# Performance work log

Hardware: AMD Instinct MI355X
Metric: run time of the kernel (lower is better)

Reference implementation:

```python
import jax, jax.numpy as jnp
import numpy as np

B, L, C, H, W = 2, 3, 64, 32, 32
DI, N, DT_RANK, K = 128, 16, 4, 4  # d_inner=2*C, d_state, dt_rank=ceil(C/16), 4 scan dirs


def setup_inputs() -> dict:
    key = jax.random.key(0)
    ks = iter(jax.random.split(key, 48))
    nrm = lambda shape, s=0.02: jax.random.normal(next(ks), shape, jnp.float32) * s
    return {
        "image_sequence": jax.random.normal(next(ks), (B, L, C, H, W), jnp.float32),
        "difficult_zone": jax.random.normal(next(ks), (B, C, H, W), jnp.float32),
        "sigma": jax.random.uniform(next(ks), (B, C, H, W), jnp.float32),
        # LayerNorm2d applied to each frame
        "norm_g": jnp.ones((C,)), "norm_b": jnp.zeros((C,)),
        # ConvolutionalResBlock (in=3C -> out=C), GroupNorm(num_groups=1)
        "gn1_g": jnp.ones((3 * C,)), "gn1_b": jnp.zeros((3 * C,)),
        "conv1_w": nrm((C, 3 * C, 3, 3)), "conv1_b": jnp.zeros((C,)),
        "gn2_g": jnp.ones((C,)), "gn2_b": jnp.zeros((C,)),
        "conv2_w": nrm((C, C, 3, 3)), "conv2_b": jnp.zeros((C,)),
        "skip_w": nrm((C, 3 * C, 1, 1)), "skip_b": jnp.zeros((C,)),
        # VSSBlock pre-norms
        "ln1_g": jnp.ones((C,)), "ln1_b": jnp.zeros((C,)),
        "ln2_g": jnp.ones((C,)), "ln2_b": jnp.zeros((C,)),
        # SS2D
        "in_proj_w": nrm((2 * DI, C)),
        "dwconv_w": nrm((DI, 1, 3, 3)), "dwconv_b": jnp.zeros((DI,)),
        "x_proj_w": nrm((K, DT_RANK + 2 * N, DI)),
        "dt_proj_w": nrm((K, DI, DT_RANK), 0.1),
        "dt_proj_b": jnp.log(jnp.expm1(jnp.full((K, DI), 0.01, jnp.float32))),
        "A_logs": jnp.log(jnp.tile(jnp.arange(1, N + 1, dtype=jnp.float32), (K * DI, 1))),
        "Ds": jnp.ones((K * DI,)),
        "out_norm_g": jnp.ones((DI,)), "out_norm_b": jnp.zeros((DI,)),
        "out_proj_w": nrm((C, DI)),
        # Mlp (hidden = C)
        "fc1_w": nrm((C, C)), "fc1_b": jnp.zeros((C,)),
        "fc2_w": nrm((C, C)), "fc2_b": jnp.zeros((C,)),
    }


def _ln(x, g, b, eps=1e-5):  # layernorm over last axis
    m = x.mean(-1, keepdims=True)
    v = x.var(-1, keepdims=True)
    return (x - m) * jax.lax.rsqrt(v + eps) * g + b


def _ln2d(x, g, b, eps=1e-6):  # per-pixel channel layernorm, NCHW
    m = x.mean(1, keepdims=True)
    v = x.var(1, keepdims=True)
    return (x - m) * jax.lax.rsqrt(v + eps) * g[None, :, None, None] + b[None, :, None, None]


def _gn1(x, g, b, eps=1e-5):  # GroupNorm(num_groups=1), NCHW
    m = x.mean((1, 2, 3), keepdims=True)
    v = x.var((1, 2, 3), keepdims=True)
    return (x - m) * jax.lax.rsqrt(v + eps) * g[None, :, None, None] + b[None, :, None, None]


def _conv(x, w, b, pad):
    y = jax.lax.conv_general_dilated(x, w, (1, 1), [(pad, pad), (pad, pad)],
                                     dimension_numbers=("NCHW", "OIHW", "NCHW"))
    return y + b[None, :, None, None]


def _forward(image_sequence, difficult_zone, sigma, norm_g, norm_b, gn1_g, gn1_b,
             conv1_w, conv1_b, gn2_g, gn2_b, conv2_w, conv2_b, skip_w, skip_b,
             ln1_g, ln1_b, ln2_g, ln2_b, in_proj_w, dwconv_w, dwconv_b, x_proj_w,
             dt_proj_w, dt_proj_b, A_logs, Ds, out_norm_g, out_norm_b, out_proj_w,
             fc1_w, fc1_b, fc2_w, fc2_b):
    b, l, c, h, w = image_sequence.shape
    bl, L2 = b * l, h * w
    # fold frame loop into batch (identical math per frame in the torch loop)
    frames = _ln2d(image_sequence.reshape(bl, c, h, w), norm_g, norm_b)
    dz = jnp.broadcast_to(difficult_zone[:, None], (b, l, c, h, w)).reshape(bl, c, h, w)
    sg = jnp.broadcast_to(sigma[:, None], (b, l, c, h, w)).reshape(bl, c, h, w)
    x = jnp.concatenate([dz, frames, sg], axis=1)  # [bl, 3c, h, w]
    # channel compressor: pre-act conv res block
    hdn = _conv(jax.nn.silu(_gn1(x, gn1_g, gn1_b)), conv1_w, conv1_b, 1)
    hdn = _conv(jax.nn.silu(_gn1(hdn, gn2_g, gn2_b)), conv2_w, conv2_b, 1)
    x = hdn + _conv(x, skip_w, skip_b, 0)          # [bl, c, h, w]
    x = x.transpose(0, 2, 3, 1)                    # [bl, h, w, c]
    # --- VSSBlock (pre-norm): x = x + SS2D(LN(x)) ---
    xn = _ln(x, ln1_g, ln1_b)
    xz = xn @ in_proj_w.T                          # [bl,h,w,2*DI]
    xc, z = jnp.split(xz, 2, axis=-1)
    xc = xc.transpose(0, 3, 1, 2)                  # [bl, DI, h, w]
    xc = jax.lax.conv_general_dilated(xc, dwconv_w, (1, 1), [(1, 1), (1, 1)],
                                      dimension_numbers=("NCHW", "OIHW", "NCHW"),
                                      feature_group_count=DI) + dwconv_b[None, :, None, None]
    xc = jax.nn.silu(xc)
    # 4-direction scan inputs (HW, WH, and their reverses)
    xf = xc.reshape(bl, DI, L2)
    xt = xc.transpose(0, 1, 3, 2).reshape(bl, DI, L2)
    xs = jnp.stack([xf, xt], axis=1)
    xs = jnp.concatenate([xs, jnp.flip(xs, axis=-1)], axis=1)  # [bl, 4, DI, L2]
    x_dbl = jnp.einsum("bkdl,kcd->bkcl", xs, x_proj_w)
    dts, Bs, Cs = jnp.split(x_dbl, [DT_RANK, DT_RANK + N], axis=2)
    dts = jnp.einsum("bkrl,kdr->bkdl", dts, dt_proj_w) + dt_proj_b[None, :, :, None]
    dts = jax.nn.softplus(dts)                     # [bl, 4, DI, L2]
    A = -jnp.exp(A_logs).reshape(K, DI, N)
    dA = jnp.exp(dts[..., None] * A[None, :, :, None, :])            # [bl,4,DI,L2,N]
    dBu = dts[..., None] * Bs.transpose(0, 1, 3, 2)[:, :, None] * xs[..., None]
    a_t = dA.transpose(3, 0, 1, 2, 4)              # [L2, bl, 4, DI, N]
    bu_t = dBu.transpose(3, 0, 1, 2, 4)
    c_t = Cs.transpose(3, 0, 1, 2)                 # [L2, bl, 4, N]

    def step(hid, inp):
        a_i, bu_i, c_i = inp
        hid = a_i * hid + bu_i
        return hid, jnp.einsum("bkdn,bkn->bkd", hid, c_i)

    h0 = jnp.zeros((bl, K, DI, N), xs.dtype)
    _, ys = jax.lax.scan(step, h0, (a_t, bu_t, c_t))                 # [L2, bl, 4, DI]
    ys = ys.transpose(1, 2, 3, 0) + xs * Ds.reshape(K, DI)[None, :, :, None]
    inv = jnp.flip(ys[:, 2:4], axis=-1)
    y = (ys[:, 0] + inv[:, 0]
         + ys[:, 1].reshape(bl, DI, w, h).transpose(0, 1, 3, 2).reshape(bl, DI, L2)
         + inv[:, 1].reshape(bl, DI, w, h).transpose(0, 1, 3, 2).reshape(bl, DI, L2))
    y = _ln(y.transpose(0, 2, 1), out_norm_g, out_norm_b).reshape(bl, h, w, DI)
    y = y * jax.nn.silu(z)
    x = x + y @ out_proj_w.T
    # --- x = x + Mlp(LN(x)) ---
    xn = _ln(x, ln2_g, ln2_b)
    x = x + (jax.nn.gelu(xn @ fc1_w.T + fc1_b, approximate=False) @ fc2_w.T + fc2_b)
    return x.transpose(0, 3, 1, 2).reshape(b, l, c, h, w)


def reference(image_sequence, difficult_zone, sigma, norm_g, norm_b, gn1_g, gn1_b,
              conv1_w, conv1_b, gn2_g, gn2_b, conv2_w, conv2_b, skip_w, skip_b,
              ln1_g, ln1_b, ln2_g, ln2_b, in_proj_w, dwconv_w, dwconv_b, x_proj_w,
              dt_proj_w, dt_proj_b, A_logs, Ds, out_norm_g, out_norm_b, out_proj_w,
              fc1_w, fc1_b, fc2_w, fc2_b):
    return _forward(image_sequence, difficult_zone, sigma, norm_g, norm_b, gn1_g, gn1_b,
                    conv1_w, conv1_b, gn2_g, gn2_b, conv2_w, conv2_b, skip_w, skip_b,
                    ln1_g, ln1_b, ln2_g, ln2_b, in_proj_w, dwconv_w, dwconv_b, x_proj_w,
                    dt_proj_w, dt_proj_b, A_logs, Ds, out_norm_g, out_norm_b, out_proj_w,
                    fc1_w, fc1_b, fc2_w, fc2_b)
```

## Files before the change

kernel.cpp:

```cpp
#include <hip/hip_runtime.h>
#include <math.h>

#define BL    6
#define CCH   64
#define C3    192
#define L2    1024
#define DIC   128
#define NST   16
#define K4    4
#define PSTR  1088
#define NCH   32

#define LOG2E 1.44269504088896340736f
#define LN2C  0.69314718055994530942f

__device__ __forceinline__ float fexp(float x){ return __builtin_amdgcn_exp2f(x*LOG2E); }
__device__ __forceinline__ float fsilu(float x){ return x / (1.f + fexp(-x)); }
__device__ __forceinline__ float fsoftplus(float x){
  if (x > 20.f) return x;
  return __builtin_amdgcn_logf(1.f + fexp(x)) * LN2C;
}
__device__ __forceinline__ float fgelu(float x){
  return 0.5f*x*(1.f + erff(x*0.70710678118654752440f));
}

__global__ __launch_bounds__(256) void k_ln2d(const float* __restrict__ img,
    const float* __restrict__ dz, const float* __restrict__ sg,
    const float* __restrict__ g, const float* __restrict__ b, float* __restrict__ x3c){
  __shared__ float ps[4][64], pq[4][64];
  int s = blockIdx.x >> 4;
  int lane = threadIdx.x & 63;
  int cg = threadIdx.x >> 6;
  int p = ((blockIdx.x & 15) << 6) + lane;
  int bsmp = s/3;
  const float* fr = img + (size_t)s*CCH*L2;
  float vals[16]; float sm=0.f, sq=0.f;
  #pragma unroll
  for (int j=0;j<16;++j){
    int c = cg*16+j;
    float v = fr[c*L2+p];
    vals[j]=v; sm+=v; sq+=v*v;
  }
  ps[cg][lane]=sm; pq[cg][lane]=sq;
  __syncthreads();
  sm = ps[0][lane]+ps[1][lane]+ps[2][lane]+ps[3][lane];
  sq = pq[0][lane]+pq[1][lane]+pq[2][lane]+pq[3][lane];
  float mean = sm*(1.f/CCH); float var = sq*(1.f/CCH) - mean*mean;
  float rs = rsqrtf(var + 1e-6f);
  float* o = x3c + (size_t)s*C3*L2;
  const float* dzp = dz + (size_t)bsmp*CCH*L2;
  const float* sgp = sg + (size_t)bsmp*CCH*L2;
  #pragma unroll
  for (int j=0;j<16;++j){
    int c = cg*16+j;
    o[c*L2+p] = dzp[c*L2+p];
    o[(CCH+c)*L2+p] = (vals[j]-mean)*rs*g[c] + b[c];
    o[(2*CCH+c)*L2+p] = sgp[c*L2+p];
  }
}

__global__ __launch_bounds__(256) void k_gnstats_part(const float* __restrict__ x,
    int elems_per_s, float* __restrict__ psum, float* __restrict__ psq){
  int s = blockIdx.x >> 4; int i = blockIdx.x & 15;
  int chunk = elems_per_s >> 4;
  int tid = threadIdx.x;
  const float* xs = x + (size_t)s*elems_per_s + (size_t)i*chunk;
  float sm=0.f, sq=0.f;
  for (int idx = tid*4; idx < chunk; idx += 1024){
    float4 v = *(const float4*)(xs+idx);
    sm += v.x+v.y+v.z+v.w;
    sq += v.x*v.x+v.y*v.y+v.z*v.z+v.w*v.w;
  }
  for (int m=1;m<64;m<<=1){ sm+=__shfl_xor(sm,m,64); sq+=__shfl_xor(sq,m,64); }
  __shared__ float s_sm[4], s_sq[4];
  int wv = tid>>6;
  if ((tid&63)==0){ s_sm[wv]=sm; s_sq[wv]=sq; }
  __syncthreads();
  if (tid==0){
    psum[s*16+i] = s_sm[0]+s_sm[1]+s_sm[2]+s_sm[3];
    psq [s*16+i] = s_sq[0]+s_sq[1]+s_sq[2]+s_sq[3];
  }
}

__global__ __launch_bounds__(64) void k_gnstats_final(const float* __restrict__ psum,
    const float* __restrict__ psq, int elems_per_s, float eps, float* __restrict__ stats){
  int s = blockIdx.x; int lane = threadIdx.x;
  float sm = lane<16 ? psum[s*16+lane] : 0.f;
  float sq = lane<16 ? psq [s*16+lane] : 0.f;
  for (int m=1;m<16;m<<=1){ sm+=__shfl_xor(sm,m,64); sq+=__shfl_xor(sq,m,64); }
  if (lane==0){
    float mean = sm/elems_per_s; float var = sq/elems_per_s - mean*mean;
    stats[s*2] = mean; stats[s*2+1] = rsqrtf(var+eps);
  }
}

__global__ __launch_bounds__(256) void k_gnact_pad(const float* __restrict__ x,
    const float* __restrict__ stats, const float* __restrict__ g, const float* __restrict__ b,
    int ch, float* __restrict__ out){
  int bx = blockIdx.x;
  int s = bx / ch; int c = bx % ch;
  int tid = threadIdx.x;
  float mean = stats[s*2], rs = stats[s*2+1];
  float gc = g[c]*rs; float bc = b[c] - mean*rs*g[c];
  float4 v = *(const float4*)(x + (size_t)bx*1024 + tid*4);
  float4 o; o.x = fsilu(v.x*gc+bc); o.y = fsilu(v.y*gc+bc);
  o.z = fsilu(v.z*gc+bc); o.w = fsilu(v.w*gc+bc);
  float* pl = out + (size_t)bx*PSTR;
  *(float4*)(pl + 32 + tid*4) = o;
  float4 z4 = make_float4(0.f,0.f,0.f,0.f);
  if (tid < 8)  *(float4*)(pl + tid*4) = z4;
  else if (tid < 16) *(float4*)(pl + 1056 + (tid-8)*4) = z4;
}

__device__ __forceinline__ void conv_row_acc(float4& a0, float4& a1, float4 mid, float lf, float rt,
    const float* wp0, const float* wp1){
  float w0=wp0[0], w1=wp0[1], w2=wp0[2];
  a0.x = fmaf(w0,lf,   fmaf(w1,mid.x, fmaf(w2,mid.y, a0.x)));
  a0.y = fmaf(w0,mid.x,fmaf(w1,mid.y, fmaf(w2,mid.z, a0.y)));
  a0.z = fmaf(w0,mid.y,fmaf(w1,mid.z, fmaf(w2,mid.w, a0.z)));
  a0.w = fmaf(w0,mid.z,fmaf(w1,mid.w, fmaf(w2,rt,    a0.w)));
  float v0=wp1[0], v1=wp1[1], v2=wp1[2];
  a1.x = fmaf(v0,lf,   fmaf(v1,mid.x, fmaf(v2,mid.y, a1.x)));
  a1.y = fmaf(v0,mid.x,fmaf(v1,mid.y, fmaf(v2,mid.z, a1.y)));
  a1.z = fmaf(v0,mid.y,fmaf(v1,mid.z, fmaf(v2,mid.w, a1.z)));
  a1.w = fmaf(v0,mid.z,fmaf(v1,mid.w, fmaf(v2,rt,    a1.w)));
}

__device__ __forceinline__ void conv_ci_body(float4 m0, float4 m1, float4 m2, int q,
    const float* wp0, const float* wp1, float4& a0, float4& a1){
  float lf0=__shfl_up(m0.w,1,64), rt0=__shfl_down(m0.x,1,64);
  float lf1=__shfl_up(m1.w,1,64), rt1=__shfl_down(m1.x,1,64);
  float lf2=__shfl_up(m2.w,1,64), rt2=__shfl_down(m2.x,1,64);
  if (q==0){ lf0=0.f; lf1=0.f; lf2=0.f; }
  if (q==7){ rt0=0.f; rt1=0.f; rt2=0.f; }
  conv_row_acc(a0,a1,m0,lf0,rt0, wp0+0, wp1+0);
  conv_row_acc(a0,a1,m1,lf1,rt1, wp0+3, wp1+3);
  conv_row_acc(a0,a1,m2,lf2,rt2, wp0+6, wp1+6);
}

__global__ __launch_bounds__(256) void k_conv1_split(const float* __restrict__ xact,
    const float* __restrict__ w, float* __restrict__ part){
  int bx = blockIdx.x; int kk = bx&7; int cop=(bx>>3)&31; int s=bx>>8;
  int co0 = cop*2, co1 = co0+1;
  int tid = threadIdx.x; int row = tid>>3; int q = tid&7; int col0 = q*4;
  float4 a0 = make_float4(0.f,0.f,0.f,0.f);
  float4 a1 = make_float4(0.f,0.f,0.f,0.f);
  int ci0 = kk*24;
  const float* pl = xact + ((size_t)s*C3 + ci0)*PSTR + row*32 + col0;
  const float* wp0 = w + (size_t)(co0*C3 + ci0)*9;
  const float* wp1 = w + (size_t)(co1*C3 + ci0)*9;
  float4 m0 = *(const float4*)(pl);
  float4 m1 = *(const float4*)(pl+32);
  float4 m2 = *(const float4*)(pl+64);
  #pragma unroll 2
  for (int i=0;i<24;++i){
    const float* pn = pl + (i<23 ? PSTR : 0);
    float4 n0 = *(const float4*)(pn);
    float4 n1 = *(const float4*)(pn+32);
    float4 n2 = *(const float4*)(pn+64);
    conv_ci_body(m0,m1,m2,q, wp0, wp1, a0, a1);
    wp0 += 9; wp1 += 9; pl = pn; m0=n0; m1=n1; m2=n2;
  }
  float* pp = part + (size_t)kk*(BL*CCH*L2) + ((size_t)s*CCH+co0)*L2 + row*32+col0;
  *(float4*)pp = a0;
  *(float4*)(pp+L2) = a1;
}

__global__ __launch_bounds__(256) void k_reduce1(const float* __restrict__ part,
    const float* __restrict__ bias, float* __restrict__ h1){
  int co = blockIdx.x & 63; int s = blockIdx.x >> 6;
  size_t ofs = ((size_t)s*CCH+co)*L2 + threadIdx.x*4;
  const size_t stride = (size_t)BL*CCH*L2;
  float4 acc = *(const float4*)(part + ofs);
  #pragma unroll
  for (int kk=1;kk<8;++kk){
    float4 r = *(const float4*)(part + (size_t)kk*stride + ofs);
    acc.x += r.x; acc.y += r.y; acc.z += r.z; acc.w += r.w;
  }
  float bv = bias[co];
  acc.x += bv; acc.y += bv; acc.z += bv; acc.w += bv;
  *(float4*)(h1 + ofs) = acc;
}

__global__ __launch_bounds__(256) void k_conv2_split(const float* __restrict__ xact2,
    const float* __restrict__ x3c, const float* __restrict__ w2,
    const float* __restrict__ wsk, float* __restrict__ part){
  int t = blockIdx.x; int role = t % 3; t /= 3;
  int cop = t & 31; int s = t >> 5;
  int co0 = cop*2, co1 = co0+1;
  int tid = threadIdx.x; int row = tid>>3; int q = tid&7; int col0 = q*4;
  int p = row*32+col0;
  float4 a0 = make_float4(0.f,0.f,0.f,0.f);
  float4 a1 = make_float4(0.f,0.f,0.f,0.f);
  if (role < 2){
    int ci0 = role*32;
    const float* pl = xact2 + ((size_t)s*CCH + ci0)*PSTR + row*32 + col0;
    const float* wp0 = w2 + (size_t)(co0*CCH + ci0)*9;
    const float* wp1 = w2 + (size_t)(co1*CCH + ci0)*9;
    float4 m0 = *(const float4*)(pl);
    float4 m1 = *(const float4*)(pl+32);
    float4 m2 = *(const float4*)(pl+64);
    #pragma unroll 2
    for (int i=0;i<32;++i){
      const float* pn = pl + (i<31 ? PSTR : 0);
      float4 n0 = *(const float4*)(pn);
      float4 n1 = *(const float4*)(pn+32);
      float4 n2 = *(const float4*)(pn+64);
      conv_ci_body(m0,m1,m2,q, wp0, wp1, a0, a1);
      wp0 += 9; wp1 += 9; pl = pn; m0=n0; m1=n1; m2=n2;
    }
  } else {
    const float* x3 = x3c + (size_t)s*C3*L2 + p;
    #pragma unroll 4
    for (int ci=0; ci<C3; ++ci){
      float4 v = *(const float4*)(x3 + (size_t)ci*L2);
      float ws0 = wsk[co0*C3+ci], ws1 = wsk[co1*C3+ci];
      a0.x = fmaf(ws0,v.x,a0.x); a0.y = fmaf(ws0,v.y,a0.y); a0.z = fmaf(ws0,v.z,a0.z); a0.w = fmaf(ws0,v.w,a0.w);
      a1.x = fmaf(ws1,v.x,a1.x); a1.y = fmaf(ws1,v.y,a1.y); a1.z = fmaf(ws1,v.z,a1.z); a1.w = fmaf(ws1,v.w,a1.w);
    }
  }
  float* pp = part + (size_t)role*(BL*CCH*L2) + ((size_t)s*CCH+co0)*L2 + p;
  *(float4*)pp = a0;
  *(float4*)(pp+L2) = a1;
}

__global__ __launch_bounds__(256) void k_reduce2(const float* __restrict__ part,
    const float* __restrict__ b2, const float* __restrict__ bsk,
    float* __restrict__ xp, float* __restrict__ x_cmaj){
  int co = blockIdx.x & 63; int s = blockIdx.x >> 6;
  int p = threadIdx.x*4;
  size_t ofs = ((size_t)s*CCH+co)*L2 + p;
  const size_t stride = (size_t)BL*CCH*L2;
  float4 r0 = *(const float4*)(part + ofs);
  float4 r1 = *(const float4*)(part + stride + ofs);
  float4 r2 = *(const float4*)(part + 2*stride + ofs);
  float bv = b2[co]+bsk[co];
  float4 o;
  o.x = r0.x+r1.x+r2.x+bv;
  o.y = r0.y+r1.y+r2.y+bv;
  o.z = r0.z+r1.z+r2.z+bv;
  o.w = r0.w+r1.w+r2.w+bv;
  *(float4*)(x_cmaj + ofs) = o;
  float* xpb = xp + ((size_t)s*L2 + p)*CCH + co;
  xpb[0] = o.x; xpb[CCH] = o.y; xpb[2*CCH] = o.z; xpb[3*CCH] = o.w;
}

__global__ __launch_bounds__(256) void k_ln1_inproj(const float* __restrict__ xp,
    const float* __restrict__ g, const float* __restrict__ b, const float* __restrict__ W,
    float* __restrict__ xc, float* __restrict__ z_t){
  __shared__ float xn_s[64*65];
  int bx = blockIdx.x; int oq = bx & 3; int pg = (bx>>2)&15; int s = bx>>6;
  int p0 = pg*64;
  int tid = threadIdx.x; int wv = __builtin_amdgcn_readfirstlane(tid>>6); int lane = tid&63;
  for (int j=0;j<16;++j){
    int pl = wv*16 + j; int p = p0 + pl;
    float v = xp[((size_t)s*L2 + p)*CCH + lane];
    float sm = v, sq = v*v;
    for (int m=1;m<64;m<<=1){ sm += __shfl_xor(sm,m,64); sq += __shfl_xor(sq,m,64); }
    float mean = sm*(1.f/64.f); float var = sq*(1.f/64.f) - mean*mean;
    float rs = rsqrtf(var + 1e-5f);
    xn_s[pl*65 + lane] = (v-mean)*rs*g[lane] + b[lane];
  }
  __syncthreads();
  int px_l = tid & 63;
  int og = __builtin_amdgcn_readfirstlane(tid >> 6);
  int o0 = oq*64 + og*16;
  float acc[16];
  #pragma unroll
  for (int oi=0;oi<16;++oi) acc[oi]=0.f;
  for (int c=0;c<64;++c){
    float xv = xn_s[px_l*65 + c];
    #pragma unroll
    for (int oi=0;oi<16;++oi) acc[oi] = fmaf(W[(o0+oi)*64 + c], xv, acc[oi]);
  }
  int p = p0 + px_l;
  if (oq < 2){
    #pragma unroll
    for (int oi=0;oi<16;++oi) xc[((size_t)s*DIC + o0 + oi)*L2 + p] = acc[oi];
  } else {
    #pragma unroll
    for (int oi=0;oi<16;++oi) z_t[((size_t)s*DIC + (o0-128) + oi)*L2 + p] = acc[oi];
  }
}

__global__ __launch_bounds__(256) void k_dwconv(const float* __restrict__ xc,
    const float* __restrict__ w, const float* __restrict__ bias, float* __restrict__ xconv){
  int bx = blockIdx.x; int dch = bx & 127; int s = bx >> 7;
  int tid = threadIdx.x; int row = tid>>3; int q = tid&7; int col0 = q*4;
  const float* xr = xc + ((size_t)s*DIC+dch)*L2;
  const float* wp = w + dch*9;
  float bv = bias[dch];
  float4 acc = make_float4(bv,bv,bv,bv);
  #pragma unroll
  for (int dy=-1;dy<=1;++dy){
    int r = row+dy;
    float4 mid = make_float4(0.f,0.f,0.f,0.f);
    if (0<=r && r<32) mid = *(const float4*)(xr + r*32 + col0);
    float lf = __shfl_up(mid.w,1,64); if(q==0) lf=0.f;
    float rt = __shfl_down(mid.x,1,64); if(q==7) rt=0.f;
    float w0=wp[(dy+1)*3], w1=wp[(dy+1)*3+1], w2=wp[(dy+1)*3+2];
    acc.x = fmaf(w0,lf,   fmaf(w1,mid.x, fmaf(w2,mid.y, acc.x)));
    acc.y = fmaf(w0,mid.x,fmaf(w1,mid.y, fmaf(w2,mid.z, acc.y)));
    acc.z = fmaf(w0,mid.y,fmaf(w1,mid.z, fmaf(w2,mid.w, acc.z)));
    acc.w = fmaf(w0,mid.z,fmaf(w1,mid.w, fmaf(w2,rt,    acc.w)));
  }
  acc.x = fsilu(acc.x); acc.y = fsilu(acc.y); acc.z = fsilu(acc.z); acc.w = fsilu(acc.w);
  *(float4*)(xconv + ((size_t)s*DIC+dch)*L2 + row*32+col0) = acc;
}

__global__ __launch_bounds__(256) void k_transp_u(const float* __restrict__ xconv,
    float* __restrict__ u_t){
  __shared__ float tb[64*65];
  int bx = blockIdx.x; int dh = bx & 1; int pg = (bx>>1)&15; int s = bx>>5;
  int tid = threadIdx.x;
  for (int i = tid; i < 64*16; i += 256){
    int dr = i>>4; int j4 = (i&15)*4;
    float4 v = *(const float4*)(xconv + ((size_t)(s*DIC + dh*64 + dr))*L2 + pg*64 + j4);
    tb[dr*65 + j4+0] = v.x; tb[dr*65 + j4+1] = v.y;
    tb[dr*65 + j4+2] = v.z; tb[dr*65 + j4+3] = v.w;
  }
  __syncthreads();
  for (int i = tid; i < 64*64; i += 256){
    int px = i>>6; int dd = i&63;
    u_t[((size_t)(s*L2) + pg*64 + px)*DIC + dh*64 + dd] = tb[dd*65 + px];
  }
}

__global__ __launch_bounds__(256) void k_xproj(const float* __restrict__ xconv,
    const float* __restrict__ W, float* __restrict__ t36){
  int bx = blockIdx.x;
  int pg = bx & 3; int t = bx >> 2;
  int cg = t % 6; int t2 = t / 6;
  int k = t2 & 3; int s = t2 >> 2;
  int px = pg*256 + threadIdx.x;
  const float* xb = xconv + (size_t)s*DIC*L2 + px;
  const float* wb = W + (size_t)(k*36 + cg*6)*DIC;
  float acc[6] = {0.f,0.f,0.f,0.f,0.f,0.f};
  for (int dch=0; dch<DIC; ++dch){
    float v = xb[(size_t)dch*L2];
    #pragma unroll
    for (int ci=0; ci<6; ++ci) acc[ci] = fmaf(wb[ci*DIC+dch], v, acc[ci]);
  }
  float* ob = t36 + ((size_t)(s*4+k)*36 + cg*6)*L2 + px;
  #pragma unroll
  for (int ci=0;ci<6;++ci) ob[(size_t)ci*L2] = acc[ci];
}

__global__ __launch_bounds__(256) void k_dt_bc(const float* __restrict__ t36,
    const float* __restrict__ dtw, const float* __restrict__ dtb,
    float* __restrict__ dtp, float* __restrict__ Bp, float* __restrict__ Cp){
  __shared__ float ld[36*68];
  int bx = blockIdx.x; int pg = bx & 15; int sk = bx >> 4;
  int k = sk & 3;
  int tid = threadIdx.x;
  const float* tbase = t36 + (size_t)sk*36*L2 + pg*64;
  for (int i = tid; i < 36*16; i += 256){
    int c = i>>4; int j4 = (i&15)*4;
    *(float4*)&ld[c*68 + j4] = *(const float4*)(tbase + (size_t)c*L2 + j4);
  }
  __syncthreads();
  int d = tid & 127; int half = tid >> 7;
  float w0 = dtw[(k*DIC+d)*4+0], w1 = dtw[(k*DIC+d)*4+1];
  float w2 = dtw[(k*DIC+d)*4+2], w3 = dtw[(k*DIC+d)*4+3];
  float bb = dtb[k*DIC+d];
  float* dout = dtp + ((size_t)sk*L2 + pg*64)*DIC + d;
  for (int pp = half*32; pp < half*32+32; ++pp){
    float r0 = ld[0*68+pp], r1 = ld[1*68+pp], r2 = ld[2*68+pp], r3 = ld[3*68+pp];
    float val = fsoftplus(fmaf(w0,r0,fmaf(w1,r1,fmaf(w2,r2,fmaf(w3,r3,bb)))));
    dout[(size_t)pp*DIC] = val;
  }
  float* Bb = Bp + ((size_t)sk*L2 + pg*64)*NST;
  float* Cb = Cp + ((size_t)sk*L2 + pg*64)*NST;
  for (int i = tid; i < 1024; i += 256){
    int pp = i>>4; int n = i&15;
    Bb[pp*NST + n] = ld[(4+n)*68 + pp];
    Cb[pp*NST + n] = ld[(20+n)*68 + pp];
  }
}

__device__ __forceinline__ int scan_pix32(int ch, int j, int k){
  if (k==0) return ch*32 + j;
  if (k==1) return j*32 + ch;
  if (k==2) return 1023 - (ch*32 + j);
  return 1023 - (j*32 + ch);
}

struct StepB { float dtv, uv; float4 B0,B1,B2,B3; };
__device__ __forceinline__ StepB loadB(const float* db, const float* ub, const float* Bb, int p){
  StepB r;
  r.dtv = db[(size_t)p*DIC]; r.uv = ub[(size_t)p*DIC];
  const float* bp = Bb + p*NST;
  r.B0 = *(const float4*)bp; r.B1 = *(const float4*)(bp+4);
  r.B2 = *(const float4*)(bp+8); r.B3 = *(const float4*)(bp+12);
  return r;
}

__global__ __launch_bounds__(256,2) void k_scan_part3(const float* __restrict__ dtp,
    const float* __restrict__ u_t, const float* __restrict__ Bp,
    const float* __restrict__ A_logs, float* __restrict__ hend, float* __restrict__ prodA){
  int bx = blockIdx.x; int chp = bx & 15; int sk = bx >> 4;
  int k = sk & 3; int s = sk >> 2;
  int tid = threadIdx.x; int d = tid & 127; int ch = chp*2 + (tid>>7);
  float aco[16];
  {
    const float* ab = A_logs + (size_t)(k*DIC+d)*NST;
    #pragma unroll
    for (int n=0;n<16;++n) aco[n] = -LOG2E * fexp(ab[n]);
  }
  float h[16], Pr[16];
  #pragma unroll
  for (int n=0;n<16;++n){ h[n]=0.f; Pr[n]=1.f; }
  const float* db = dtp + (size_t)sk*L2*DIC + d;
  const float* ub = u_t + (size_t)s*L2*DIC + d;
  const float* Bb = Bp + (size_t)sk*L2*NST;
  StepB cur = loadB(db, ub, Bb, scan_pix32(ch, 0, k));
  #pragma unroll 4
  for (int j=0;j<32;++j){
    StepB nxt;
    if (j < 31) nxt = loadB(db, ub, Bb, scan_pix32(ch, j+1, k));
    float tv = cur.dtv*cur.uv;
    #define PSTEP(NI, BV) { float a_ = __builtin_amdgcn_exp2f(cur.dtv*aco[NI]); \
      h[NI] = fmaf(a_, h[NI], tv*(BV)); Pr[NI] *= a_; }
    PSTEP(0,cur.B0.x) PSTEP(1,cur.B0.y) PSTEP(2,cur.B0.z) PSTEP(3,cur.B0.w)
    PSTEP(4,cur.B1.x) PSTEP(5,cur.B1.y) PSTEP(6,cur.B1.z) PSTEP(7,cur.B1.w)
    PSTEP(8,cur.B2.x) PSTEP(9,cur.B2.y) PSTEP(10,cur.B2.z) PSTEP(11,cur.B2.w)
    PSTEP(12,cur.B3.x) PSTEP(13,cur.B3.y) PSTEP(14,cur.B3.z) PSTEP(15,cur.B3.w)
    #undef PSTEP
    cur = nxt;
  }
  size_t base = ((size_t)(sk*NCH + ch)*DIC + d)*NST;
  #pragma unroll
  for (int q4=0;q4<4;++q4){
    *(float4*)(hend + base + q4*4)  = make_float4(h[q4*4],h[q4*4+1],h[q4*4+2],h[q4*4+3]);
    *(float4*)(prodA + base + q4*4) = make_float4(Pr[q4*4],Pr[q4*4+1],Pr[q4*4+2],Pr[q4*4+3]);
  }
}

__global__ __launch_bounds__(256) void k_scan_fix3(const float* __restrict__ hend,
    float* prodA_Hin){
  int t = blockIdx.x*256 + threadIdx.x;
  int n = t & 15; int d = (t>>4) & 127; int sk = t >> 11;
  float H = 0.f;
  for (int ch=0; ch<NCH; ++ch){
    size_t idx = ((size_t)(sk*NCH + ch)*DIC + d)*NST + n;
    float pa = prodA_Hin[idx];
    float he = hend[idx];
    prodA_Hin[idx] = H;
    H = fmaf(pa, H, he);
  }
}

__global__ __launch_bounds__(256,2) void k_scan_y3(const float* __restrict__ dtp,
    const float* __restrict__ u_t, const float* __restrict__ Bp, const float* __restrict__ Cp,
    const float* __restrict__ A_logs, const float* __restrict__ Ds,
    const float* __restrict__ Hin, float* __restrict__ ys_t){
  int bx = blockIdx.x; int chp = bx & 15; int sk = bx >> 4;
  int k = sk & 3; int s = sk >> 2;
  int tid = threadIdx.x; int d = tid & 127; int ch = chp*2 + (tid>>7);
  float aco[16];
  {
    const float* ab = A_logs + (size_t)(k*DIC+d)*NST;
    #pragma unroll
    for (int n=0;n<16;++n) aco[n] = -LOG2E * fexp(ab[n]);
  }
  float Dv = Ds[k*DIC+d];
  float h[16];
  size_t hbase = ((size_t)(sk*NCH + ch)*DIC + d)*NST;
  #pragma unroll
  for (int q4=0;q4<4;++q4){
    float4 hv = *(const float4*)(Hin + hbase + q4*4);
    h[q4*4]=hv.x; h[q4*4+1]=hv.y; h[q4*4+2]=hv.z; h[q4*4+3]=hv.w;
  }
  const float* db = dtp + (size_t)sk*L2*DIC + d;
  const float* ub = u_t + (size_t)s*L2*DIC + d;
  const float* Bb = Bp + (size_t)sk*L2*NST;
  const float* Cb = Cp + (size_t)sk*L2*NST;
  float* yb = ys_t + (size_t)sk*L2*DIC + d;
  int pcur = scan_pix32(ch, 0, k);
  StepB cur = loadB(db, ub, Bb, pcur);
  float4 Cc0 = *(const float4*)(Cb + pcur*NST);
  float4 Cc1 = *(const float4*)(Cb + pcur*NST + 4);
  float4 Cc2 = *(const float4*)(Cb + pcur*NST + 8);
  float4 Cc3 = *(const float4*)(Cb + pcur*NST + 12);
  #pragma unroll 4
  for (int j=0;j<32;++j){
    StepB nxt; float4 Cn0, Cn1, Cn2, Cn3; int pn = pcur;
    if (j < 31){
      pn = scan_pix32(ch, j+1, k);
      nxt = loadB(db, ub, Bb, pn);
      Cn0 = *(const float4*)(Cb + pn*NST);
      Cn1 = *(const float4*)(Cb + pn*NST + 4);
      Cn2 = *(const float4*)(Cb + pn*NST + 8);
      Cn3 = *(const float4*)(Cb + pn*NST + 12);
    }
    float tv = cur.dtv*cur.uv;
    float y0=0.f, y1=0.f, y2=0.f, y3=0.f;
    #define YSTEP(NI, BV, CV, YA) { float a_ = __builtin_amdgcn_exp2f(cur.dtv*aco[NI]); \
      h[NI] = fmaf(a_, h[NI], tv*(BV)); YA = fmaf(h[NI], (CV), YA); }
    YSTEP(0,cur.B0.x,Cc0.x,y0) YSTEP(1,cur.B0.y,Cc0.y,y1) YSTEP(2,cur.B0.z,Cc0.z,y2) YSTEP(3,cur.B0.w,Cc0.w,y3)
    YSTEP(4,cur.B1.x,Cc1.x,y0) YSTEP(5,cur.B1.y,Cc1.y,y1) YSTEP(6,cur.B1.z,Cc1.z,y2) YSTEP(7,cur.B1.w,Cc1.w,y3)
    YSTEP(8,cur.B2.x,Cc2.x,y0) YSTEP(9,cur.B2.y,Cc2.y,y1) YSTEP(10,cur.B2.z,Cc2.z,y2) YSTEP(11,cur.B2.w,Cc2.w,y3)
    YSTEP(12,cur.B3.x,Cc3.x,y0) YSTEP(13,cur.B3.y,Cc3.y,y1) YSTEP(14,cur.B3.z,Cc3.z,y2) YSTEP(15,cur.B3.w,Cc3.w,y3)
    #undef YSTEP
    yb[(size_t)pcur*DIC] = fmaf(cur.uv, Dv, (y0+y1)+(y2+y3));
    cur = nxt; Cc0 = Cn0; Cc1 = Cn1; Cc2 = Cn2; Cc3 = Cn3; pcur = pn;
  }
}

__global__ __launch_bounds__(256) void k_combine2(const float* __restrict__ ys_t,
    const float* __restrict__ z_t, const float* __restrict__ g, const float* __restrict__ b,
    float* __restrict__ yf){
  __shared__ float yt[128*65];
  int s = blockIdx.x >> 4; int pg = blockIdx.x & 15;
  int tid = threadIdx.x;
  int wv = __builtin_amdgcn_readfirstlane(tid>>6); int lane = tid&63;
  int d0 = lane, d1 = lane+64;
  for (int i=0;i<16;++i){
    int px = i*4 + wv; int p = pg*64 + px;
    const float* yb = ys_t + ((size_t)(s*4)*L2 + p)*DIC;
    float ya = yb[d0] + yb[(size_t)L2*DIC + d0] + yb[(size_t)2*L2*DIC + d0] + yb[(size_t)3*L2*DIC + d0];
    float yc = yb[d1] + yb[(size_t)L2*DIC + d1] + yb[(size_t)2*L2*DIC + d1] + yb[(size_t)3*L2*DIC + d1];
    float sm = ya+yc, sq = ya*ya+yc*yc;
    for (int m=1;m<64;m<<=1){ sm+=__shfl_xor(sm,m,64); sq+=__shfl_xor(sq,m,64); }
    float mean = sm*(1.f/128.f); float var = sq*(1.f/128.f)-mean*mean;
    float rs = rsqrtf(var + 1e-5f);
    float yn0 = (ya-mean)*rs*g[d0] + b[d0];
    float yn1 = (yc-mean)*rs*g[d1] + b[d1];
    float zv0 = z_t[((size_t)s*DIC+d0)*L2 + p];
    float zv1 = z_t[((size_t)s*DIC+d1)*L2 + p];
    yt[d0*65 + px] = yn0 * fsilu(zv0);
    yt[d1*65 + px] = yn1 * fsilu(zv1);
  }
  __syncthreads();
  for (int idx = tid; idx < 128*64; idx += 256){
    int r = idx>>6; int jj = idx&63;
    yf[((size_t)s*DIC + r)*L2 + pg*64 + jj] = yt[r*65 + jj];
  }
}

__global__ __launch_bounds__(256) void k_outproj(const float* __restrict__ yf,
    const float* __restrict__ x_cmaj, const float* __restrict__ W, float* __restrict__ xv){
  int bx = blockIdx.x; int cb = bx&3; int pg=(bx>>2)&15; int s=bx>>6;
  int lane = threadIdx.x&63;
  int cq = __builtin_amdgcn_readfirstlane(threadIdx.x>>6);
  int px = pg*64 + lane; int c0 = cb*16 + cq*4;
  const float* yb = yf + (size_t)s*DIC*L2 + px;
  float a0=0.f,a1=0.f,a2=0.f,a3=0.f;
  for (int dch=0;dch<DIC;++dch){
    float v = yb[(size_t)dch*L2];
    a0 = fmaf(W[(c0+0)*DIC+dch], v, a0);
    a1 = fmaf(W[(c0+1)*DIC+dch], v, a1);
    a2 = fmaf(W[(c0+2)*DIC+dch], v, a2);
    a3 = fmaf(W[(c0+3)*DIC+dch], v, a3);
  }
  size_t base = ((size_t)s*CCH+c0)*L2 + px;
  xv[base]        = x_cmaj[base]        + a0;
  xv[base+L2]     = x_cmaj[base+L2]     + a1;
  xv[base+2*L2]   = x_cmaj[base+2*L2]   + a2;
  xv[base+3*L2]   = x_cmaj[base+3*L2]   + a3;
}

__global__ __launch_bounds__(256) void k_mlp(const float* __restrict__ xv_in,
    const float* __restrict__ g, const float* __restrict__ b,
    const float* __restrict__ w1, const float* __restrict__ b1,
    const float* __restrict__ w2, const float* __restrict__ b2, float* __restrict__ out){
  __shared__ float xt[64*65];
  __shared__ float ts[64*65];
  int s = blockIdx.x >> 4; int p0 = (blockIdx.x & 15)*64;
  int tid = threadIdx.x; int lane = tid & 63;
  int grp = __builtin_amdgcn_readfirstlane(tid >> 6);
  for (int j=0;j<16;++j){
    int c = grp*16 + j;
    xt[c*65 + lane] = xv_in[((size_t)s*CCH + c)*L2 + p0 + lane];
  }
  __syncthreads();
  float sm=0.f, sq=0.f;
  for (int c=0;c<64;++c){ float v = xt[c*65+lane]; sm+=v; sq+=v*v; }
  float mean = sm*(1.f/64.f);
  float rs = rsqrtf(sq*(1.f/64.f) - mean*mean + 1e-5f);
  int o0 = grp*16;
  float t[16];
  #pragma unroll
  for (int oi=0;oi<16;++oi) t[oi] = b1[o0+oi];
  for (int c=0;c<64;++c){
    float xn = (xt[c*65+lane]-mean)*rs*g[c] + b[c];
    #pragma unroll
    for (int oi=0;oi<16;++oi) t[oi] = fmaf(xn, w1[(o0+oi)*64 + c], t[oi]);
  }
  #pragma unroll
  for (int oi=0;oi<16;++oi) ts[lane*65 + o0+oi] = fgelu(t[oi]);
  __syncthreads();
  int c0 = grp*16;
  float acc[16];
  #pragma unroll
  for (int ci=0;ci<16;++ci) acc[ci] = xt[(c0+ci)*65+lane] + b2[c0+ci];
  for (int o=0;o<64;++o){
    float tv = ts[lane*65 + o];
    #pragma unroll
    for (int ci=0;ci<16;++ci) acc[ci] = fmaf(tv, w2[(c0+ci)*64 + o], acc[ci]);
  }
  #pragma unroll
  for (int ci=0;ci<16;++ci) out[((size_t)s*CCH + c0+ci)*L2 + p0 + lane] = acc[ci];
}

extern "C" void kernel_launch(void* const* d_in, const int* in_sizes, int n_in,
                              void* d_out, int out_size, void* d_ws, size_t ws_size,
                              hipStream_t stream){
  (void)in_sizes; (void)n_in; (void)out_size; (void)ws_size;
  const float* img      = (const float*)d_in[0];
  const float* dz       = (const float*)d_in[1];
  const float* sg       = (const float*)d_in[2];
  const float* norm_g   = (const float*)d_in[3];
  const float* norm_b   = (const float*)d_in[4];
  const float* gn1_g    = (const float*)d_in[5];
  const float* gn1_b    = (const float*)d_in[6];
  const float* conv1_w  = (const float*)d_in[7];
  const float* conv1_b  = (const float*)d_in[8];
  const float* gn2_g    = (const float*)d_in[9];
  const float* gn2_b    = (const float*)d_in[10];
  const float* conv2_w  = (const float*)d_in[11];
  const float* conv2_b  = (const float*)d_in[12];
  const float* skip_w   = (const float*)d_in[13];
  const float* skip_b   = (const float*)d_in[14];
  const float* ln1_g    = (const float*)d_in[15];
  const float* ln1_b    = (const float*)d_in[16];
  const float* ln2_g    = (const float*)d_in[17];
  const float* ln2_b    = (const float*)d_in[18];
  const float* in_proj_w= (const float*)d_in[19];
  const float* dwconv_w = (const float*)d_in[20];
  const float* dwconv_b = (const float*)d_in[21];
  const float* x_proj_w = (const float*)d_in[22];
  const float* dt_proj_w= (const float*)d_in[23];
  const float* dt_proj_b= (const float*)d_in[24];
  const float* A_logs   = (const float*)d_in[25];
  const float* Ds       = (const float*)d_in[26];
  const float* out_norm_g = (const float*)d_in[27];
  const float* out_norm_b = (const float*)d_in[28];
  const float* out_proj_w = (const float*)d_in[29];
  const float* fc1_w    = (const float*)d_in[30];
  const float* fc1_b    = (const float*)d_in[31];
  const float* fc2_w    = (const float*)d_in[32];
  const float* fc2_b    = (const float*)d_in[33];

  float* ws = (float*)d_ws;
  float* x3c    = ws;
  float* xact1  = x3c    + 1179648;
  float* h1     = xact1  + 1253376;
  float* xact2  = h1     + 393216;
  float* xp     = xact2  + 417792;
  float* x_cmaj = xp     + 393216;
  float* z_t    = x_cmaj + 393216;
  float* xc     = z_t    + 786432;
  float* xconv  = xc     + 786432;
  float* t36    = xconv  + 786432;
  float* dtp    = t36    + 884736;
  float* ys_t   = dtp    + 3145728;
  float* yf     = ys_t   + 3145728;
  float* xv     = yf     + 786432;
  float* psum   = xv     + 393216;
  float* psq    = psum   + 96;
  float* stats1 = psq    + 96;
  float* stats2 = stats1 + 12;
  float* part1  = dtp;
  float* part2  = ys_t;
  float* hend   = x3c;
  float* prodA  = xconv;
  float* u_t    = h1;
  float* Bp     = xp;
  float* Cp     = xc;

  k_ln2d<<<96, 256, 0, stream>>>(img, dz, sg, norm_g, norm_b, x3c);
  k_gnstats_part<<<96, 256, 0, stream>>>(x3c, C3*L2, psum, psq);
  k_gnstats_final<<<6, 64, 0, stream>>>(psum, psq, C3*L2, 1e-5f, stats1);
  k_gnact_pad<<<6*C3, 256, 0, stream>>>(x3c, stats1, gn1_g, gn1_b, C3, xact1);
  k_conv1_split<<<1536, 256, 0, stream>>>(xact1, conv1_w, part1);
  k_reduce1<<<384, 256, 0, stream>>>(part1, conv1_b, h1);
  k_gnstats_part<<<96, 256, 0, stream>>>(h1, CCH*L2, psum, psq);
  k_gnstats_final<<<6, 64, 0, stream>>>(psum, psq, CCH*L2, 1e-5f, stats2);
  k_gnact_pad<<<6*CCH, 256, 0, stream>>>(h1, stats2, gn2_g, gn2_b, CCH, xact2);
  k_conv2_split<<<576, 256, 0, stream>>>(xact2, x3c, conv2_w, skip_w, part2);
  k_reduce2<<<384, 256, 0, stream>>>(part2, conv2_b, skip_b, xp, x_cmaj);
  k_ln1_inproj<<<384, 256, 0, stream>>>(xp, ln1_g, ln1_b, in_proj_w, xc, z_t);
  k_dwconv<<<768, 256, 0, stream>>>(xc, dwconv_w, dwconv_b, xconv);
  k_transp_u<<<192, 256, 0, stream>>>(xconv, u_t);
  k_xproj<<<576, 256, 0, stream>>>(xconv, x_proj_w, t36);
  k_dt_bc<<<384, 256, 0, stream>>>(t36, dt_proj_w, dt_proj_b, dtp, Bp, Cp);
  k_scan_part3<<<384, 256, 0, stream>>>(dtp, u_t, Bp, A_logs, hend, prodA);
  k_scan_fix3<<<192, 256, 0, stream>>>(hend, prodA);
  k_scan_y3<<<384, 256, 0, stream>>>(dtp, u_t, Bp, Cp, A_logs, Ds, prodA, ys_t);
  k_combine2<<<96, 256, 0, stream>>>(ys_t, z_t, out_norm_g, out_norm_b, yf);
  k_outproj<<<384, 256, 0, stream>>>(yf, x_cmaj, out_proj_w, xv);
  k_mlp<<<96, 256, 0, stream>>>(xv, ln2_g, ln2_b, fc1_w, fc1_b, fc2_w, fc2_b, (float*)d_out);
}
```

Baseline: 344.4 us.

## Fuse GroupNorm stats into producers and merge xproj/dt and combine/outproj kernels

GroupNorm statistics are now accumulated with atomics inside k_ln2d and k_reduce1, which removes four separate stats kernels and a re-read of x3c and h1. x_proj is fused with the dt/B/C projection through shared memory, which drops the t36 intermediate. The combine/out-norm step is fused with out_proj, which drops the yf intermediate. This cuts launches and global traffic. In exchange it adds a memset, float atomics whose summation order is nondeterministic, and larger shared-memory tiles.

```diff
diff --git a/kernel.cpp b/kernel.cpp
--- a/kernel.cpp
+++ b/kernel.cpp
@@ -26,7 +26,8 @@
 
 __global__ __launch_bounds__(256) void k_ln2d(const float* __restrict__ img,
     const float* __restrict__ dz, const float* __restrict__ sg,
-    const float* __restrict__ g, const float* __restrict__ b, float* __restrict__ x3c){
+    const float* __restrict__ g, const float* __restrict__ b, float* __restrict__ x3c,
+    float* __restrict__ psum1, float* __restrict__ psq1){
   __shared__ float ps[4][64], pq[4][64];
   int s = blockIdx.x >> 4;
   int lane = threadIdx.x & 63;
@@ -50,57 +51,38 @@
   float* o = x3c + (size_t)s*C3*L2;
   const float* dzp = dz + (size_t)bsmp*CCH*L2;
   const float* sgp = sg + (size_t)bsmp*CCH*L2;
+  float gsm=0.f, gsq=0.f;
   #pragma unroll
   for (int j=0;j<16;++j){
     int c = cg*16+j;
-    o[c*L2+p] = dzp[c*L2+p];
-    o[(CCH+c)*L2+p] = (vals[j]-mean)*rs*g[c] + b[c];
-    o[(2*CCH+c)*L2+p] = sgp[c*L2+p];
-  }
-}
-
-__global__ __launch_bounds__(256) void k_gnstats_part(const float* __restrict__ x,
-    int elems_per_s, float* __restrict__ psum, float* __restrict__ psq){
-  int s = blockIdx.x >> 4; int i = blockIdx.x & 15;
-  int chunk = elems_per_s >> 4;
-  int tid = threadIdx.x;
-  const float* xs = x + (size_t)s*elems_per_s + (size_t)i*chunk;
-  float sm=0.f, sq=0.f;
-  for (int idx = tid*4; idx < chunk; idx += 1024){
-    float4 v = *(const float4*)(xs+idx);
-    sm += v.x+v.y+v.z+v.w;
-    sq += v.x*v.x+v.y*v.y+v.z*v.z+v.w*v.w;
-  }
-  for (int m=1;m<64;m<<=1){ sm+=__shfl_xor(sm,m,64); sq+=__shfl_xor(sq,m,64); }
-  __shared__ float s_sm[4], s_sq[4];
-  int wv = tid>>6;
-  if ((tid&63)==0){ s_sm[wv]=sm; s_sq[wv]=sq; }
-  __syncthreads();
-  if (tid==0){
-    psum[s*16+i] = s_sm[0]+s_sm[1]+s_sm[2]+s_sm[3];
-    psq [s*16+i] = s_sq[0]+s_sq[1]+s_sq[2]+s_sq[3];
-  }
-}
-
-__global__ __launch_bounds__(64) void k_gnstats_final(const float* __restrict__ psum,
-    const float* __restrict__ psq, int elems_per_s, float eps, float* __restrict__ stats){
-  int s = blockIdx.x; int lane = threadIdx.x;
-  float sm = lane<16 ? psum[s*16+lane] : 0.f;
-  float sq = lane<16 ? psq [s*16+lane] : 0.f;
-  for (int m=1;m<16;m<<=1){ sm+=__shfl_xor(sm,m,64); sq+=__shfl_xor(sq,m,64); }
-  if (lane==0){
-    float mean = sm/elems_per_s; float var = sq/elems_per_s - mean*mean;
-    stats[s*2] = mean; stats[s*2+1] = rsqrtf(var+eps);
+    float dzv = dzp[c*L2+p];
+    float nv  = (vals[j]-mean)*rs*g[c] + b[c];
+    float sgv = sgp[c*L2+p];
+    o[c*L2+p] = dzv;
+    o[(CCH+c)*L2+p] = nv;
+    o[(2*CCH+c)*L2+p] = sgv;
+    gsm += dzv+nv+sgv; gsq += dzv*dzv+nv*nv+sgv*sgv;
+  }
+  for (int m=1;m<64;m<<=1){ gsm+=__shfl_xor(gsm,m,64); gsq+=__shfl_xor(gsq,m,64); }
+  __syncthreads();
+  if (lane==0){ ps[cg][0]=gsm; pq[cg][0]=gsq; }
+  __syncthreads();
+  if (threadIdx.x==0){
+    atomicAdd(psum1+s, ps[0][0]+ps[1][0]+ps[2][0]+ps[3][0]);
+    atomicAdd(psq1 +s, pq[0][0]+pq[1][0]+pq[2][0]+pq[3][0]);
   }
 }
 
 __global__ __launch_bounds__(256) void k_gnact_pad(const float* __restrict__ x,
-    const float* __restrict__ stats, const float* __restrict__ g, const float* __restrict__ b,
-    int ch, float* __restrict__ out){
+    const float* __restrict__ psum, const float* __restrict__ psq,
+    const float* __restrict__ g, const float* __restrict__ b,
+    int ch, float inv_n, float eps, float* __restrict__ out){
   int bx = blockIdx.x;
   int s = bx / ch; int c = bx % ch;
   int tid = threadIdx.x;
-  float mean = stats[s*2], rs = stats[s*2+1];
+  float mean = psum[s]*inv_n;
+  float var = psq[s]*inv_n - mean*mean;
+  float rs = rsqrtf(var + eps);
   float gc = g[c]*rs; float bc = b[c] - mean*rs*g[c];
   float4 v = *(const float4*)(x + (size_t)bx*1024 + tid*4);
   float4 o; o.x = fsilu(v.x*gc+bc); o.y = fsilu(v.y*gc+bc);
@@ -167,7 +149,8 @@
 }
 
 __global__ __launch_bounds__(256) void k_reduce1(const float* __restrict__ part,
-    const float* __restrict__ bias, float* __restrict__ h1){
+    const float* __restrict__ bias, float* __restrict__ h1,
+    float* __restrict__ psum2, float* __restrict__ psq2){
   int co = blockIdx.x & 63; int s = blockIdx.x >> 6;
   size_t ofs = ((size_t)s*CCH+co)*L2 + threadIdx.x*4;
   const size_t stride = (size_t)BL*CCH*L2;
@@ -180,6 +163,17 @@
   float bv = bias[co];
   acc.x += bv; acc.y += bv; acc.z += bv; acc.w += bv;
   *(float4*)(h1 + ofs) = acc;
+  float sm = acc.x+acc.y+acc.z+acc.w;
+  float sq = acc.x*acc.x+acc.y*acc.y+acc.z*acc.z+acc.w*acc.w;
+  for (int m=1;m<64;m<<=1){ sm+=__shfl_xor(sm,m,64); sq+=__shfl_xor(sq,m,64); }
+  __shared__ float s_sm[4], s_sq[4];
+  int wv = threadIdx.x>>6;
+  if ((threadIdx.x&63)==0){ s_sm[wv]=sm; s_sq[wv]=sq; }
+  __syncthreads();
+  if (threadIdx.x==0){
+    atomicAdd(psum2+s, s_sm[0]+s_sm[1]+s_sm[2]+s_sm[3]);
+    atomicAdd(psq2 +s, s_sq[0]+s_sq[1]+s_sq[2]+s_sq[3]);
+  }
 }
 
 __global__ __launch_bounds__(256) void k_conv2_split(const float* __restrict__ xact2,
@@ -326,38 +320,34 @@
   }
 }
 
-__global__ __launch_bounds__(256) void k_xproj(const float* __restrict__ xconv,
-    const float* __restrict__ W, float* __restrict__ t36){
-  int bx = blockIdx.x;
-  int pg = bx & 3; int t = bx >> 2;
-  int cg = t % 6; int t2 = t / 6;
-  int k = t2 & 3; int s = t2 >> 2;
-  int px = pg*256 + threadIdx.x;
-  const float* xb = xconv + (size_t)s*DIC*L2 + px;
-  const float* wb = W + (size_t)(k*36 + cg*6)*DIC;
-  float acc[6] = {0.f,0.f,0.f,0.f,0.f,0.f};
-  for (int dch=0; dch<DIC; ++dch){
-    float v = xb[(size_t)dch*L2];
-    #pragma unroll
-    for (int ci=0; ci<6; ++ci) acc[ci] = fmaf(wb[ci*DIC+dch], v, acc[ci]);
-  }
-  float* ob = t36 + ((size_t)(s*4+k)*36 + cg*6)*L2 + px;
-  #pragma unroll
-  for (int ci=0;ci<6;++ci) ob[(size_t)ci*L2] = acc[ci];
-}
-
-__global__ __launch_bounds__(256) void k_dt_bc(const float* __restrict__ t36,
-    const float* __restrict__ dtw, const float* __restrict__ dtb,
+__global__ __launch_bounds__(256) void k_xproj_dt(const float* __restrict__ xconv,
+    const float* __restrict__ W, const float* __restrict__ dtw, const float* __restrict__ dtb,
     float* __restrict__ dtp, float* __restrict__ Bp, float* __restrict__ Cp){
-  __shared__ float ld[36*68];
+  __shared__ float smem[128*68];
   int bx = blockIdx.x; int pg = bx & 15; int sk = bx >> 4;
-  int k = sk & 3;
+  int k = sk & 3; int s = sk >> 2;
   int tid = threadIdx.x;
-  const float* tbase = t36 + (size_t)sk*36*L2 + pg*64;
-  for (int i = tid; i < 36*16; i += 256){
-    int c = i>>4; int j4 = (i&15)*4;
-    *(float4*)&ld[c*68 + j4] = *(const float4*)(tbase + (size_t)c*L2 + j4);
-  }
+  for (int i = tid; i < 128*16; i += 256){
+    int dr = i>>4; int j4 = (i&15)*4;
+    float4 v = *(const float4*)(xconv + ((size_t)(s*DIC + dr))*L2 + pg*64 + j4);
+    *(float4*)&smem[dr*68 + j4] = v;
+  }
+  __syncthreads();
+  int px = tid & 63;
+  int cgrp = __builtin_amdgcn_readfirstlane(tid >> 6);
+  int c0 = cgrp*9;
+  const float* wb = W + (size_t)(k*36 + c0)*DIC;
+  float acc[9];
+  #pragma unroll
+  for (int ci=0;ci<9;++ci) acc[ci]=0.f;
+  for (int d=0; d<DIC; ++d){
+    float xv = smem[d*68 + px];
+    #pragma unroll
+    for (int ci=0;ci<9;++ci) acc[ci] = fmaf(wb[ci*DIC+d], xv, acc[ci]);
+  }
+  __syncthreads();
+  #pragma unroll
+  for (int ci=0;ci<9;++ci) smem[(c0+ci)*68 + px] = acc[ci];
   __syncthreads();
   int d = tid & 127; int half = tid >> 7;
   float w0 = dtw[(k*DIC+d)*4+0], w1 = dtw[(k*DIC+d)*4+1];
@@ -365,7 +355,7 @@
   float bb = dtb[k*DIC+d];
   float* dout = dtp + ((size_t)sk*L2 + pg*64)*DIC + d;
   for (int pp = half*32; pp < half*32+32; ++pp){
-    float r0 = ld[0*68+pp], r1 = ld[1*68+pp], r2 = ld[2*68+pp], r3 = ld[3*68+pp];
+    float r0 = smem[0*68+pp], r1 = smem[1*68+pp], r2 = smem[2*68+pp], r3 = smem[3*68+pp];
     float val = fsoftplus(fmaf(w0,r0,fmaf(w1,r1,fmaf(w2,r2,fmaf(w3,r3,bb)))));
     dout[(size_t)pp*DIC] = val;
   }
@@ -373,8 +363,8 @@
   float* Cb = Cp + ((size_t)sk*L2 + pg*64)*NST;
   for (int i = tid; i < 1024; i += 256){
     int pp = i>>4; int n = i&15;
-    Bb[pp*NST + n] = ld[(4+n)*68 + pp];
-    Cb[pp*NST + n] = ld[(20+n)*68 + pp];
+    Bb[pp*NST + n] = smem[(4+n)*68 + pp];
+    Cb[pp*NST + n] = smem[(20+n)*68 + pp];
   }
 }
 
@@ -507,16 +497,16 @@
   }
 }
 
-__global__ __launch_bounds__(256) void k_combine2(const float* __restrict__ ys_t,
+__global__ __launch_bounds__(256) void k_combine_outproj(const float* __restrict__ ys_t,
     const float* __restrict__ z_t, const float* __restrict__ g, const float* __restrict__ b,
-    float* __restrict__ yf){
-  __shared__ float yt[128*65];
-  int s = blockIdx.x >> 4; int pg = blockIdx.x & 15;
+    const float* __restrict__ W, const float* __restrict__ x_cmaj, float* __restrict__ xv){
+  __shared__ float yt[128*33];
+  int s = blockIdx.x >> 5; int pg = blockIdx.x & 31;
   int tid = threadIdx.x;
   int wv = __builtin_amdgcn_readfirstlane(tid>>6); int lane = tid&63;
   int d0 = lane, d1 = lane+64;
-  for (int i=0;i<16;++i){
-    int px = i*4 + wv; int p = pg*64 + px;
+  for (int i=0;i<8;++i){
+    int px = i*4 + wv; int p = pg*32 + px;
     const float* yb = ys_t + ((size_t)(s*4)*L2 + p)*DIC;
     float ya = yb[d0] + yb[(size_t)L2*DIC + d0] + yb[(size_t)2*L2*DIC + d0] + yb[(size_t)3*L2*DIC + d0];
     float yc = yb[d1] + yb[(size_t)L2*DIC + d1] + yb[(size_t)2*L2*DIC + d1] + yb[(size_t)3*L2*DIC + d1];
@@ -528,36 +518,26 @@
     float yn1 = (yc-mean)*rs*g[d1] + b[d1];
     float zv0 = z_t[((size_t)s*DIC+d0)*L2 + p];
     float zv1 = z_t[((size_t)s*DIC+d1)*L2 + p];
-    yt[d0*65 + px] = yn0 * fsilu(zv0);
-    yt[d1*65 + px] = yn1 * fsilu(zv1);
-  }
-  __syncthreads();
-  for (int idx = tid; idx < 128*64; idx += 256){
-    int r = idx>>6; int jj = idx&63;
-    yf[((size_t)s*DIC + r)*L2 + pg*64 + jj] = yt[r*65 + jj];
-  }
-}
-
-__global__ __launch_bounds__(256) void k_outproj(const float* __restrict__ yf,
-    const float* __restrict__ x_cmaj, const float* __restrict__ W, float* __restrict__ xv){
-  int bx = blockIdx.x; int cb = bx&3; int pg=(bx>>2)&15; int s=bx>>6;
-  int lane = threadIdx.x&63;
-  int cq = __builtin_amdgcn_readfirstlane(threadIdx.x>>6);
-  int px = pg*64 + lane; int c0 = cb*16 + cq*4;
-  const float* yb = yf + (size_t)s*DIC*L2 + px;
-  float a0=0.f,a1=0.f,a2=0.f,a3=0.f;
-  for (int dch=0;dch<DIC;++dch){
-    float v = yb[(size_t)dch*L2];
-    a0 = fmaf(W[(c0+0)*DIC+dch], v, a0);
-    a1 = fmaf(W[(c0+1)*DIC+dch], v, a1);
-    a2 = fmaf(W[(c0+2)*DIC+dch], v, a2);
-    a3 = fmaf(W[(c0+3)*DIC+dch], v, a3);
-  }
-  size_t base = ((size_t)s*CCH+c0)*L2 + px;
-  xv[base]        = x_cmaj[base]        + a0;
-  xv[base+L2]     = x_cmaj[base+L2]     + a1;
-  xv[base+2*L2]   = x_cmaj[base+2*L2]   + a2;
-  xv[base+3*L2]   = x_cmaj[base+3*L2]   + a3;
+    yt[d0*33 + px] = yn0 * fsilu(zv0);
+    yt[d1*33 + px] = yn1 * fsilu(zv1);
+  }
+  __syncthreads();
+  int px = tid & 31; int cg = tid >> 5;
+  int c0 = cg*8;
+  float acc[8];
+  #pragma unroll
+  for (int ci=0;ci<8;++ci) acc[ci]=0.f;
+  for (int d=0; d<DIC; ++d){
+    float yv = yt[d*33 + px];
+    #pragma unroll
+    for (int ci=0;ci<8;++ci) acc[ci] = fmaf(W[(c0+ci)*DIC + d], yv, acc[ci]);
+  }
+  int p = pg*32 + px;
+  #pragma unroll
+  for (int ci=0;ci<8;++ci){
+    size_t base = ((size_t)s*CCH + c0+ci)*L2 + p;
+    xv[base] = x_cmaj[base] + acc[ci];
+  }
 }
 
 __global__ __launch_bounds__(256) void k_mlp(const float* __restrict__ xv_in,
@@ -652,15 +632,15 @@
   float* z_t    = x_cmaj + 393216;
   float* xc     = z_t    + 786432;
   float* xconv  = xc     + 786432;
-  float* t36    = xconv  + 786432;
-  float* dtp    = t36    + 884736;
+  float* hole   = xconv  + 786432;
+  float* dtp    = hole   + 884736;
   float* ys_t   = dtp    + 3145728;
-  float* yf     = ys_t   + 3145728;
-  float* xv     = yf     + 786432;
-  float* psum   = xv     + 393216;
-  float* psq    = psum   + 96;
-  float* stats1 = psq    + 96;
-  float* stats2 = stats1 + 12;
+  float* xv     = ys_t   + 3145728;
+  float* statsb = xv     + 393216;
+  float* psum1  = statsb;
+  float* psq1   = statsb + 6;
+  float* psum2  = statsb + 12;
+  float* psq2   = statsb + 18;
   float* part1  = dtp;
   float* part2  = ys_t;
   float* hend   = x3c;
@@ -669,26 +649,24 @@
   float* Bp     = xp;
   float* Cp     = xc;
 
-  k_ln2d<<<96, 256, 0, stream>>>(img, dz, sg, norm_g, norm_b, x3c);
-  k_gnstats_part<<<96, 256, 0, stream>>>(x3c, C3*L2, psum, psq);
-  k_gnstats_final<<<6, 64, 0, stream>>>(psum, psq, C3*L2, 1e-5f, stats1);
-  k_gnact_pad<<<6*C3, 256, 0, stream>>>(x3c, stats1, gn1_g, gn1_b, C3, xact1);
+  hipMemsetAsync(statsb, 0, 24*sizeof(float), stream);
+  k_ln2d<<<96, 256, 0, stream>>>(img, dz, sg, norm_g, norm_b, x3c, psum1, psq1);
+  k_gnact_pad<<<6*C3, 256, 0, stream>>>(x3c, psum1, psq1, gn1_g, gn1_b, C3,
+                                        1.f/(C3*L2), 1e-5f, xact1);
   k_conv1_split<<<1536, 256, 0, stream>>>(xact1, conv1_w, part1);
-  k_reduce1<<<384, 256, 0, stream>>>(part1, conv1_b, h1);
-  k_gnstats_part<<<96, 256, 0, stream>>>(h1, CCH*L2, psum, psq);
-  k_gnstats_final<<<6, 64, 0, stream>>>(psum, psq, CCH*L2, 1e-5f, stats2);
-  k_gnact_pad<<<6*CCH, 256, 0, stream>>>(h1, stats2, gn2_g, gn2_b, CCH, xact2);
+  k_reduce1<<<384, 256, 0, stream>>>(part1, conv1_b, h1, psum2, psq2);
+  k_gnact_pad<<<6*CCH, 256, 0, stream>>>(h1, psum2, psq2, gn2_g, gn2_b, CCH,
+                                         1.f/(CCH*L2), 1e-5f, xact2);
   k_conv2_split<<<576, 256, 0, stream>>>(xact2, x3c, conv2_w, skip_w, part2);
   k_reduce2<<<384, 256, 0, stream>>>(part2, conv2_b, skip_b, xp, x_cmaj);
   k_ln1_inproj<<<384, 256, 0, stream>>>(xp, ln1_g, ln1_b, in_proj_w, xc, z_t);
   k_dwconv<<<768, 256, 0, stream>>>(xc, dwconv_w, dwconv_b, xconv);
   k_transp_u<<<192, 256, 0, stream>>>(xconv, u_t);
-  k_xproj<<<576, 256, 0, stream>>>(xconv, x_proj_w, t36);
-  k_dt_bc<<<384, 256, 0, stream>>>(t36, dt_proj_w, dt_proj_b, dtp, Bp, Cp);
+  k_xproj_dt<<<384, 256, 0, stream>>>(xconv, x_proj_w, dt_proj_w, dt_proj_b, dtp, Bp, Cp);
   k_scan_part3<<<384, 256, 0, stream>>>(dtp, u_t, Bp, A_logs, hend, prodA);
   k_scan_fix3<<<192, 256, 0, stream>>>(hend, prodA);
   k_scan_y3<<<384, 256, 0, stream>>>(dtp, u_t, Bp, Cp, A_logs, Ds, prodA, ys_t);
-  k_combine2<<<96, 256, 0, stream>>>(ys_t, z_t, out_norm_g, out_norm_b, yf);
-  k_outproj<<<384, 256, 0, stream>>>(yf, x_cmaj, out_proj_w, xv);
+  k_combine_outproj<<<192, 256, 0, stream>>>(ys_t, z_t, out_norm_g, out_norm_b,
+                                             out_proj_w, x_cmaj, xv);
   k_mlp<<<96, 256, 0, stream>>>(xv, ln2_g, ln2_b, fc1_w, fc1_b, fc2_w, fc2_b, (float*)d_out);
 }
```

Measured after the change: 326.7 us. 1.05x faster.
